# Kernel optimization log

Hardware: AMD Instinct MI355X
Metric: run time of the kernel (lower is better)

## Reference

```python
import jax, jax.numpy as jnp
import numpy as np

N_NODES = 65536
N_EDGES = 524288
N_GRAPHS = 512
G_NODES = 10000
NUM_DISEASES = 2000
IN_DIM = 128
HID = 256  # 2 * IN_DIM (z_emb concat feat)
D_FEAT = 512
C_FEAT = 512
MAX_Z = 4000


def setup_inputs() -> dict:
    key = jax.random.key(0)
    ks = jax.random.split(key, 20)
    rn = lambda k, shape: jax.random.normal(k, shape, dtype=jnp.float32) * 0.05
    return {
        "z": jax.random.randint(ks[0], (N_NODES,), 0, MAX_Z),
        "node_id": jnp.sort(jax.random.randint(ks[1], (N_NODES,), 0, G_NODES)),
        "src": jax.random.randint(ks[2], (N_EDGES,), 0, N_NODES),
        "dst": jax.random.randint(ks[3], (N_EDGES,), 0, N_NODES),
        "graph_ids": jnp.sort(jax.random.randint(ks[4], (N_NODES,), 0, N_GRAPHS)),
        "z_table": rn(ks[5], (MAX_Z, IN_DIM)),
        "d_feat_tab": rn(ks[6], (G_NODES, D_FEAT)),
        "c_feat_tab": rn(ks[7], (G_NODES, C_FEAT)),
        "Wd": rn(ks[8], (D_FEAT, IN_DIM)),
        "Wc": rn(ks[9], (C_FEAT, IN_DIM)),
        "gin_W1": rn(ks[10], (HID, HID)), "gin_b1": jnp.zeros((HID,), jnp.float32),
        "gin_W2": rn(ks[11], (HID, HID)), "gin_b2": jnp.zeros((HID,), jnp.float32),
        "sage_Wself": rn(ks[12], (HID, HID)),
        "sage_Wneigh": rn(ks[13], (HID, HID)),
        "sage_b": jnp.zeros((HID,), jnp.float32),
        "lin1_W": rn(ks[14], (HID, HID)), "lin1_b": jnp.zeros((HID,), jnp.float32),
        "lin2_W": rn(ks[15], (HID, 1)), "lin2_b": jnp.zeros((1,), jnp.float32),
    }


def reference(z, node_id, src, dst, graph_ids, z_table, d_feat_tab, c_feat_tab,
              Wd, Wc, gin_W1, gin_b1, gin_W2, gin_b2,
              sage_Wself, sage_Wneigh, sage_b, lin1_W, lin1_b, lin2_W, lin2_b):
    # --- input feature construction (Model.forward) ---
    z_emb = z_table[z]                               # [N, IN_DIM]
    d_proj = d_feat_tab[node_id] @ Wd                # d_fc (bias=False)
    c_proj = c_feat_tab[node_id] @ Wc                # c_fc (bias=False)
    disease = (node_id <= NUM_DISEASES)[:, None]
    # node_id is sorted -> masked concat order == node order
    feat = jnp.where(disease, d_proj, c_proj)        # [N, IN_DIM]
    x = jnp.concatenate([z_emb, feat], axis=1)       # [N, HID]
    # --- GINConv: sum aggregation, eps=0, mlp = Lin->ReLU->Lin ---
    agg = jax.ops.segment_sum(x[src], dst, num_segments=N_NODES)
    h = x + agg
    h = jax.nn.relu(h @ gin_W1 + gin_b1) @ gin_W2 + gin_b2
    # --- SAGEConv('mean'): fc_self(h) + fc_neigh(mean_neighbors) + bias ---
    deg = jax.ops.segment_sum(jnp.ones((N_EDGES,), h.dtype), dst, num_segments=N_NODES)
    mean_n = jax.ops.segment_sum(h[src], dst, num_segments=N_NODES) / jnp.maximum(deg, 1.0)[:, None]
    h = h @ sage_Wself + mean_n @ sage_Wneigh + sage_b
    # --- per-graph max pooling readout ---
    g = jax.ops.segment_max(h, graph_ids, num_segments=N_GRAPHS, indices_are_sorted=True)
    g = jnp.where(jnp.isfinite(g), g, 0.0)           # guard empty graphs
    # --- head: Linear -> ReLU -> (dropout p=0, eval) -> Linear ---
    h = jax.nn.relu(g @ lin1_W + lin1_b)
    return h @ lin2_W + lin2_b                       # [N_GRAPHS, 1]
```

## Files before the change

### kernel.cpp

```cpp
#include <hip/hip_runtime.h>
#include <hip/hip_bf16.h>

#define N_NODES     65536
#define N_EDGES     524288
#define N_GRAPHS    512
#define G_NODES_N   10000
#define NUM_DIS     2000
#define IN_DIM      128
#define HID         256
#define D_FEAT      512
#define MAX_Z       4000
#define POOL_SPLIT  8

typedef _Float16 half8 __attribute__((ext_vector_type(8)));
typedef float    f32x4 __attribute__((ext_vector_type(4)));

typedef __attribute__((address_space(1))) const void as1_void;
typedef __attribute__((address_space(3))) void       as3_void;

__global__ __launch_bounds__(256) void prep_kernel(
    const float* __restrict__ Ws, const float* __restrict__ Wn,
    const float* __restrict__ Wd, const float* __restrict__ Wc,
    const float* __restrict__ W1, const float* __restrict__ W2,
    const float* __restrict__ z_table,
    const int* __restrict__ z, const int* __restrict__ node_id,
    _Float16* __restrict__ WsT, _Float16* __restrict__ WnT,
    _Float16* __restrict__ WdT, _Float16* __restrict__ WcT,
    _Float16* __restrict__ W12P, _Float16* __restrict__ zt16,
    int2* __restrict__ zn2, int* __restrict__ cnt, int* __restrict__ flags)
{
    const int b = blockIdx.x;
    const int tid = threadIdx.x;
    if (b < 64) {
        __shared__ float tile[64][65];
        const float* W; _Float16* T; int K, N, k0, n0;
        if (b < 32) {
            const int mat = b >> 4, t = b & 15;
            K = HID; N = HID; k0 = (t >> 2) * 64; n0 = (t & 3) * 64;
            W = (mat == 0) ? Ws : Wn;
            T = (mat == 0) ? WsT : WnT;
        } else {
            const int bb = b - 32;
            const int mat = bb >> 4, t = bb & 15;
            K = D_FEAT; N = IN_DIM; k0 = (t >> 1) * 64; n0 = (t & 1) * 64;
            W = (mat == 0) ? Wd : Wc;
            T = (mat == 0) ? WdT : WcT;
        }
        const int tx = tid & 63, ty = tid >> 6;
        #pragma unroll
        for (int r = 0; r < 64; r += 4)
            tile[r + ty][tx] = W[(size_t)(k0 + r + ty) * N + n0 + tx];
        __syncthreads();
        #pragma unroll
        for (int c = 0; c < 64; c += 4)
            T[(size_t)(n0 + c + ty) * K + k0 + tx] = (_Float16)tile[tx][c + ty];
    } else if (b < 576) {
        const int bb = b - 64;
        const int mat = bb >> 8;
        const int k = bb & 255;
        const int n = tid;
        const float* W = mat ? W2 : W1;
        const float v = W[(size_t)k * HID + n];
        const size_t idx = (size_t)(mat * 8 + (k >> 5)) * 8192
                         + (size_t)((((k >> 3) & 3) * 256 + n) * 8 + (k & 7));
        W12P[idx] = (_Float16)v;
    } else if (b < 826) {
        const size_t base = ((size_t)(b - 576) * 256 + tid) * 8;
        const float4 f0 = *(const float4*)(z_table + base);
        const float4 f1 = *(const float4*)(z_table + base + 4);
        half8 h;
        h[0]=(_Float16)f0.x; h[1]=(_Float16)f0.y; h[2]=(_Float16)f0.z; h[3]=(_Float16)f0.w;
        h[4]=(_Float16)f1.x; h[5]=(_Float16)f1.y; h[6]=(_Float16)f1.z; h[7]=(_Float16)f1.w;
        *(half8*)(zt16 + base) = h;
    } else if (b < 890) {
        const int base = (b - 826) * 1024 + tid * 4;
        *(int4*)(cnt + base) = make_int4(0, 0, 0, 0);
        if (b == 826 && tid < 128) flags[tid] = 0;
    } else {
        const int i = (b - 890) * 256 + tid;
        zn2[i] = make_int2(z[i], node_id[i]);
    }
}

__global__ __launch_bounds__(256) void proj_hist_kernel(
    const float* __restrict__ dtab, const float* __restrict__ ctab,
    const _Float16* __restrict__ WdT, const _Float16* __restrict__ WcT,
    _Float16* __restrict__ proj,
    const int* __restrict__ dst, int* __restrict__ cnt)
{
    const int blk = blockIdx.x;
    if (blk >= 79) {
        const int e = (blk - 79) * 256 + threadIdx.x;
        if (e < N_EDGES) atomicAdd(&cnt[dst[e]], 1);
        return;
    }
    __shared__ _Float16 Alds[128 * 40];
    __shared__ _Float16 Blds[128 * 40];
    const float* tab; const _Float16* WT; int base, M, bm;
    if (blk < 16) { tab = dtab; WT = WdT; base = 0;           M = NUM_DIS + 1;             bm = blk * 128; }
    else          { tab = ctab; WT = WcT; base = NUM_DIS + 1; M = G_NODES_N - NUM_DIS - 1; bm = (blk - 16) * 128; }
    const int tid  = threadIdx.x;
    const int wave = tid >> 6, lane = tid & 63;
    const int q    = lane >> 4, l16 = lane & 15;
    const int mbase = (wave & 1) * 64, nbase = (wave >> 1) * 64;
    const int r = tid >> 1, s = tid & 1;

    f32x4 acc[4][4] = {};

    for (int kc = 0; kc < 16; ++kc) {
        const int k0 = kc * 32;
        const int arow = min(bm + r, M - 1);
        const float* gA = tab + (size_t)(base + arow) * D_FEAT + k0 + s * 16;
        const _Float16* gB = WT + (size_t)r * D_FEAT + k0 + s * 16;
        const float4 f0 = ((const float4*)gA)[0];
        const float4 f1 = ((const float4*)gA)[1];
        const float4 f2 = ((const float4*)gA)[2];
        const float4 f3 = ((const float4*)gA)[3];
        const half8 hb0 = *(const half8*)gB;
        const half8 hb1 = *(const half8*)(gB + 8);
        half8 h0, h1;
        h0[0]=(_Float16)f0.x; h0[1]=(_Float16)f0.y; h0[2]=(_Float16)f0.z; h0[3]=(_Float16)f0.w;
        h0[4]=(_Float16)f1.x; h0[5]=(_Float16)f1.y; h0[6]=(_Float16)f1.z; h0[7]=(_Float16)f1.w;
        h1[0]=(_Float16)f2.x; h1[1]=(_Float16)f2.y; h1[2]=(_Float16)f2.z; h1[3]=(_Float16)f2.w;
        h1[4]=(_Float16)f3.x; h1[5]=(_Float16)f3.y; h1[6]=(_Float16)f3.z; h1[7]=(_Float16)f3.w;
        __syncthreads();
        *(half8*)&Alds[r * 40 + s * 16]     = h0;
        *(half8*)&Alds[r * 40 + s * 16 + 8] = h1;
        *(half8*)&Blds[r * 40 + s * 16]     = hb0;
        *(half8*)&Blds[r * 40 + s * 16 + 8] = hb1;
        __syncthreads();
        half8 a[4], b[4];
        #pragma unroll
        for (int i = 0; i < 4; ++i)
            a[i] = *(const half8*)&Alds[(mbase + i * 16 + l16) * 40 + q * 8];
        #pragma unroll
        for (int j = 0; j < 4; ++j)
            b[j] = *(const half8*)&Blds[(nbase + j * 16 + l16) * 40 + q * 8];
        #pragma unroll
        for (int i = 0; i < 4; ++i)
            #pragma unroll
            for (int j = 0; j < 4; ++j)
                acc[i][j] = __builtin_amdgcn_mfma_f32_16x16x32_f16(a[i], b[j], acc[i][j], 0, 0, 0);
    }

    #pragma unroll
    for (int j = 0; j < 4; ++j) {
        const int colg = nbase + j * 16 + l16;
        #pragma unroll
        for (int i = 0; i < 4; ++i) {
            #pragma unroll
            for (int rr = 0; rr < 4; ++rr) {
                const int row = bm + mbase + i * 16 + q * 4 + rr;
                if (row < M)
                    proj[(size_t)(base + row) * IN_DIM + colg] = (_Float16)acc[i][j][rr];
            }
        }
    }
}

__global__ __launch_bounds__(256) void scan_fused_kernel(
    const int* __restrict__ cnt, int* __restrict__ row_ptr,
    int* __restrict__ fill, int* __restrict__ flags)
{
    __shared__ int a[256], b[256];
    __shared__ int sums[64];
    __shared__ int segbase;
    const int t = threadIdx.x;
    const int blk = blockIdx.x;
    const int base = blk * 1024 + t * 4;
    const int4 c = *(const int4*)(cnt + base);
    const int s = c.x + c.y + c.z + c.w;
    a[t] = s;
    __syncthreads();
    int* in = a; int* out = b;
    for (int off = 1; off < 256; off <<= 1) {
        out[t] = in[t] + ((t >= off) ? in[t - off] : 0);
        __syncthreads();
        int* tmp = in; in = out; out = tmp;
    }
    if (t == 0) {
        atomicExch(&flags[64 + blk], in[255]);
        __threadfence();
        atomicAdd(&flags[0], 1);
        while (atomicAdd(&flags[0], 0) < 64) {}
    }
    __syncthreads();
    if (t < 64) sums[t] = atomicAdd(&flags[64 + t], 0);
    __syncthreads();
    if (t == 0) {
        int pfx = 0;
        for (int i = 0; i < blk; ++i) pfx += sums[i];
        segbase = pfx;
        if (blk == 63) {
            int tot = pfx;
            for (int i = blk; i < 64; ++i) tot += sums[i];
            row_ptr[N_NODES] = tot;
        }
    }
    __syncthreads();
    const int run = in[t] - s + segbase;
    int4 r;
    r.x = run; r.y = run + c.x; r.z = r.y + c.y; r.w = r.z + c.z;
    *(int4*)(row_ptr + base) = r;
    *(int4*)(fill + base) = r;
}

__global__ __launch_bounds__(256) void scatter_kernel(
    const int* __restrict__ src, const int* __restrict__ dst,
    const int2* __restrict__ zn2,
    int* __restrict__ fill, int* __restrict__ col, int2* __restrict__ colzn)
{
    const int e = blockIdx.x * 256 + threadIdx.x;
    if (e < N_EDGES) {
        const int s = src[e];
        const int pos = atomicAdd(&fill[dst[e]], 1);
        col[pos] = s;
        colzn[pos] = zn2[s];
    }
}

__global__ __launch_bounds__(256) void gin_fused_kernel(
    const int* __restrict__ row_ptr, const int2* __restrict__ colzn,
    const int2* __restrict__ zn2,
    const _Float16* __restrict__ zt16, const _Float16* __restrict__ proj,
    const _Float16* __restrict__ W12P,
    const float* __restrict__ b1, const float* __restrict__ b2,
    _Float16* __restrict__ H)
{
    __shared__ _Float16 Apanel[64 * 264];
    __shared__ _Float16 Blds[8192];

    const int bm   = blockIdx.x * 64;
    const int tid  = threadIdx.x;
    const int wave = tid >> 6, lane = tid & 63;
    const int q    = lane >> 4, l16 = lane & 15;
    const int nbase = wave * 64;

    auto stage = [&](int c) {
        const _Float16* src = W12P + (size_t)c * 8192;
        #pragma unroll
        for (int tt = 0; tt < 4; ++tt) {
            const int seg = (wave * 4 + tt) * 64 + lane;
            __builtin_amdgcn_global_load_lds((as1_void*)(src + seg * 8),
                (as3_void*)&Blds[(wave * 4 + tt) * 64 * 8], 16, 0, 0);
        }
    };

    stage(0);

    {
        const int p = tid & 7;
        #pragma unroll 1
        for (int pass = 0; pass < 2; ++pass) {
            const int r  = (tid >> 3) + (pass << 5);
            const int gr = bm + r;
            const int beg = row_ptr[gr], end = row_ptr[gr + 1];
            float za[16], pa[16];
            {
                const int2 zn = zn2[gr];
                const half8* zp = (const half8*)(zt16 + (size_t)zn.x * IN_DIM + p * 16);
                const half8* pp = (const half8*)(proj + (size_t)zn.y * IN_DIM + p * 16);
                const half8 z0 = zp[0], z1 = zp[1], p0 = pp[0], p1 = pp[1];
                #pragma unroll
                for (int i = 0; i < 8; ++i) {
                    za[i] = (float)z0[i]; za[8 + i] = (float)z1[i];
                    pa[i] = (float)p0[i]; pa[8 + i] = (float)p1[i];
                }
            }
            int e = beg;
            for (; e + 4 <= end; e += 4) {
                const int2 znA = colzn[e],     znB = colzn[e + 1];
                const int2 znC = colzn[e + 2], znD = colzn[e + 3];
                const half8* zpA = (const half8*)(zt16 + (size_t)znA.x * IN_DIM + p * 16);
                const half8* ppA = (const half8*)(proj + (size_t)znA.y * IN_DIM + p * 16);
                const half8* zpB = (const half8*)(zt16 + (size_t)znB.x * IN_DIM + p * 16);
                const half8* ppB = (const half8*)(proj + (size_t)znB.y * IN_DIM + p * 16);
                const half8* zpC = (const half8*)(zt16 + (size_t)znC.x * IN_DIM + p * 16);
                const half8* ppC = (const half8*)(proj + (size_t)znC.y * IN_DIM + p * 16);
                const half8* zpD = (const half8*)(zt16 + (size_t)znD.x * IN_DIM + p * 16);
                const half8* ppD = (const half8*)(proj + (size_t)znD.y * IN_DIM + p * 16);
                const half8 zA0 = zpA[0], zA1 = zpA[1], pA0 = ppA[0], pA1 = ppA[1];
                const half8 zB0 = zpB[0], zB1 = zpB[1], pB0 = ppB[0], pB1 = ppB[1];
                const half8 zC0 = zpC[0], zC1 = zpC[1], pC0 = ppC[0], pC1 = ppC[1];
                const half8 zD0 = zpD[0], zD1 = zpD[1], pD0 = ppD[0], pD1 = ppD[1];
                #pragma unroll
                for (int i = 0; i < 8; ++i) {
                    za[i]     += ((float)zA0[i] + (float)zB0[i]) + ((float)zC0[i] + (float)zD0[i]);
                    za[8 + i] += ((float)zA1[i] + (float)zB1[i]) + ((float)zC1[i] + (float)zD1[i]);
                    pa[i]     += ((float)pA0[i] + (float)pB0[i]) + ((float)pC0[i] + (float)pD0[i]);
                    pa[8 + i] += ((float)pA1[i] + (float)pB1[i]) + ((float)pC1[i] + (float)pD1[i]);
                }
            }
            for (; e + 2 <= end; e += 2) {
                const int2 znA = colzn[e];
                const int2 znB = colzn[e + 1];
                const half8* zpA = (const half8*)(zt16 + (size_t)znA.x * IN_DIM + p * 16);
                const half8* ppA = (const half8*)(proj + (size_t)znA.y * IN_DIM + p * 16);
                const half8* zpB = (const half8*)(zt16 + (size_t)znB.x * IN_DIM + p * 16);
                const half8* ppB = (const half8*)(proj + (size_t)znB.y * IN_DIM + p * 16);
                const half8 zA0 = zpA[0], zA1 = zpA[1], pA0 = ppA[0], pA1 = ppA[1];
                const half8 zB0 = zpB[0], zB1 = zpB[1], pB0 = ppB[0], pB1 = ppB[1];
                #pragma unroll
                for (int i = 0; i < 8; ++i) {
                    za[i]     += (float)zA0[i] + (float)zB0[i];
                    za[8 + i] += (float)zA1[i] + (float)zB1[i];
                    pa[i]     += (float)pA0[i] + (float)pB0[i];
                    pa[8 + i] += (float)pA1[i] + (float)pB1[i];
                }
            }
            if (e < end) {
                const int2 zn = colzn[e];
                const half8* zp = (const half8*)(zt16 + (size_t)zn.x * IN_DIM + p * 16);
                const half8* pp = (const half8*)(proj + (size_t)zn.y * IN_DIM + p * 16);
                const half8 z0 = zp[0], z1 = zp[1], p0 = pp[0], p1 = pp[1];
                #pragma unroll
                for (int i = 0; i < 8; ++i) {
                    za[i] += (float)z0[i]; za[8 + i] += (float)z1[i];
                    pa[i] += (float)p0[i]; pa[8 + i] += (float)p1[i];
                }
            }
            half8 oz0, oz1, op0, op1;
            #pragma unroll
            for (int i = 0; i < 8; ++i) {
                oz0[i] = (_Float16)za[i];     oz1[i] = (_Float16)za[8 + i];
                op0[i] = (_Float16)pa[i];     op1[i] = (_Float16)pa[8 + i];
            }
            *(half8*)&Apanel[r * 264 + p * 16]           = oz0;
            *(half8*)&Apanel[r * 264 + p * 16 + 8]       = oz1;
            *(half8*)&Apanel[r * 264 + 128 + p * 16]     = op0;
            *(half8*)&Apanel[r * 264 + 128 + p * 16 + 8] = op1;
        }
    }
    __syncthreads();

    f32x4 acc[4][4] = {};
    for (int c = 0; c < 16; ++c) {
        if (c) {
            __syncthreads();
            stage(c);
            if (c == 8) {
                #pragma unroll
                for (int j = 0; j < 4; ++j) {
                    const int colg = nbase + j * 16 + l16;
                    const float bv = b1[colg];
                    #pragma unroll
                    for (int i = 0; i < 4; ++i)
                        #pragma unroll
                        for (int rr = 0; rr < 4; ++rr) {
                            const float v = fmaxf(acc[i][j][rr] + bv, 0.0f);
                            Apanel[(i * 16 + q * 4 + rr) * 264 + colg] = (_Float16)v;
                            acc[i][j][rr] = 0.0f;
                        }
                }
            }
            __syncthreads();
        }
        const int kl = (c & 7) * 32;
        half8 a[4], b[4];
        #pragma unroll
        for (int i = 0; i < 4; ++i)
            a[i] = *(const half8*)&Apanel[(i * 16 + l16) * 264 + kl + q * 8];
        #pragma unroll
        for (int j = 0; j < 4; ++j)
            b[j] = *(const half8*)&Blds[(q * 256 + nbase + j * 16 + l16) * 8];
        #pragma unroll
        for (int i = 0; i < 4; ++i)
            #pragma unroll
            for (int j = 0; j < 4; ++j)
                acc[i][j] = __builtin_amdgcn_mfma_f32_16x16x32_f16(a[i], b[j], acc[i][j], 0, 0, 0);
    }

    #pragma unroll
    for (int j = 0; j < 4; ++j) {
        const int colg = nbase + j * 16 + l16;
        const float bv = b2[colg];
        #pragma unroll
        for (int i = 0; i < 4; ++i)
            #pragma unroll
            for (int rr = 0; rr < 4; ++rr) {
                const int rowg = bm + i * 16 + q * 4 + rr;
                H[(size_t)rowg * HID + colg] = (_Float16)(acc[i][j][rr] + bv);
            }
    }
}

__global__ __launch_bounds__(256) void csr_agg_kernel(
    const int* __restrict__ row_ptr, const int* __restrict__ col,
    const _Float16* __restrict__ F, _Float16* __restrict__ OUT)
{
    const int t = blockIdx.x * 256 + threadIdx.x;
    const int d = t >> 5;
    const int q = t & 31;
    const int beg = row_ptr[d];
    const int end = row_ptr[d + 1];
    float acc[8] = {0.f,0.f,0.f,0.f,0.f,0.f,0.f,0.f};
    int e = beg;
    for (; e + 8 <= end; e += 8) {
        const int s0 = col[e],     s1 = col[e + 1];
        const int s2 = col[e + 2], s3 = col[e + 3];
        const int s4 = col[e + 4], s5 = col[e + 5];
        const int s6 = col[e + 6], s7 = col[e + 7];
        const half8 v0 = *(const half8*)(F + (size_t)s0 * HID + q * 8);
        const half8 v1 = *(const half8*)(F + (size_t)s1 * HID + q * 8);
        const half8 v2 = *(const half8*)(F + (size_t)s2 * HID + q * 8);
        const half8 v3 = *(const half8*)(F + (size_t)s3 * HID + q * 8);
        const half8 v4 = *(const half8*)(F + (size_t)s4 * HID + q * 8);
        const half8 v5 = *(const half8*)(F + (size_t)s5 * HID + q * 8);
        const half8 v6 = *(const half8*)(F + (size_t)s6 * HID + q * 8);
        const half8 v7 = *(const half8*)(F + (size_t)s7 * HID + q * 8);
        #pragma unroll
        for (int i = 0; i < 8; ++i)
            acc[i] += (((float)v0[i] + (float)v1[i]) + ((float)v2[i] + (float)v3[i]))
                    + (((float)v4[i] + (float)v5[i]) + ((float)v6[i] + (float)v7[i]));
    }
    for (; e + 4 <= end; e += 4) {
        const int s0 = col[e],     s1 = col[e + 1];
        const int s2 = col[e + 2], s3 = col[e + 3];
        const half8 v0 = *(const half8*)(F + (size_t)s0 * HID + q * 8);
        const half8 v1 = *(const half8*)(F + (size_t)s1 * HID + q * 8);
        const half8 v2 = *(const half8*)(F + (size_t)s2 * HID + q * 8);
        const half8 v3 = *(const half8*)(F + (size_t)s3 * HID + q * 8);
        #pragma unroll
        for (int i = 0; i < 8; ++i)
            acc[i] += ((float)v0[i] + (float)v1[i]) + ((float)v2[i] + (float)v3[i]);
    }
    for (; e < end; ++e) {
        const half8 v0 = *(const half8*)(F + (size_t)col[e] * HID + q * 8);
        #pragma unroll
        for (int i = 0; i < 8; ++i) acc[i] += (float)v0[i];
    }
    const float rs = 1.0f / fmaxf((float)(end - beg), 1.0f);
    half8 o;
    #pragma unroll
    for (int i = 0; i < 8; ++i) o[i] = (_Float16)(acc[i] * rs);
    *(half8*)(OUT + (size_t)d * HID + q * 8) = o;
}

__global__ __launch_bounds__(256) void mfma_gemm_kernel(
    const _Float16* __restrict__ A1, const _Float16* __restrict__ A2,
    const _Float16* __restrict__ B1T, const _Float16* __restrict__ B2T,
    const float* __restrict__ bias, _Float16* __restrict__ Ch)
{
    __shared__ _Float16 Alds[128 * 32];
    __shared__ _Float16 Blds[128 * 32];
    const int bm   = blockIdx.x * 128;
    const int bn   = blockIdx.y * 128;
    const int tid  = threadIdx.x;
    const int wave = tid >> 6, lane = tid & 63;
    const int q    = lane >> 4, l16 = lane & 15;
    const int mbase = (wave & 1) * 64, nbase = (wave >> 1) * 64;

    f32x4 acc[4][4] = {};

    for (int kc = 0; kc < 16; ++kc) {
        const int k0 = (kc & 7) * 32;
        const _Float16* Abase = (kc < 8) ? A1 : A2;
        const _Float16* Bbase = (kc < 8) ? B1T : B2T;
        __syncthreads();
        #pragma unroll
        for (int t = 0; t < 2; ++t) {
            const int i   = wave * 128 + t * 64 + lane;
            const int row = i >> 2, s = i & 3;
            const _Float16* gA = Abase + (size_t)(bm + row) * HID + k0 + s * 8;
            const _Float16* gB = Bbase + (size_t)(bn + row) * HID + k0 + s * 8;
            __builtin_amdgcn_global_load_lds(
                (as1_void*)gA, (as3_void*)&Alds[(wave * 128 + t * 64) * 8], 16, 0, 0);
            __builtin_amdgcn_global_load_lds(
                (as1_void*)gB, (as3_void*)&Blds[(wave * 128 + t * 64) * 8], 16, 0, 0);
        }
        __syncthreads();
        half8 a[4], b[4];
        #pragma unroll
        for (int i = 0; i < 4; ++i)
            a[i] = *(const half8*)&Alds[(mbase + i * 16 + l16) * 32 + q * 8];
        #pragma unroll
        for (int j = 0; j < 4; ++j)
            b[j] = *(const half8*)&Blds[(nbase + j * 16 + l16) * 32 + q * 8];
        #pragma unroll
        for (int i = 0; i < 4; ++i)
            #pragma unroll
            for (int j = 0; j < 4; ++j)
                acc[i][j] = __builtin_amdgcn_mfma_f32_16x16x32_f16(a[i], b[j], acc[i][j], 0, 0, 0);
    }

    #pragma unroll
    for (int j = 0; j < 4; ++j) {
        const int colg = bn + nbase + j * 16 + l16;
        const float bv = bias[colg];
        #pragma unroll
        for (int i = 0; i < 4; ++i) {
            #pragma unroll
            for (int rr = 0; rr < 4; ++rr) {
                const int rowg = bm + mbase + i * 16 + q * 4 + rr;
                Ch[(size_t)rowg * HID + colg] = (_Float16)(acc[i][j][rr] + bv);
            }
        }
    }
}

__global__ __launch_bounds__(256) void pool_part_kernel(
    const _Float16* __restrict__ H2, const int* __restrict__ gid,
    float* __restrict__ Gpart)
{
    const int g = blockIdx.y;
    const int sp = blockIdx.x;
    const int j = threadIdx.x;
    int lo = 0, hi = N_NODES;
    while (lo < hi) { const int mid = (lo + hi) >> 1; if (gid[mid] < g) lo = mid + 1; else hi = mid; }
    const int start = lo;
    hi = N_NODES;
    while (lo < hi) { const int mid = (lo + hi) >> 1; if (gid[mid] < g + 1) lo = mid + 1; else hi = mid; }
    const int end = lo;
    float m = -INFINITY;
    for (int i = start + sp; i < end; i += POOL_SPLIT)
        m = fmaxf(m, (float)H2[(size_t)i * HID + j]);
    Gpart[((size_t)g * POOL_SPLIT + sp) * HID + j] = m;
}

__global__ __launch_bounds__(256) void head_kernel(
    const float* __restrict__ Gpart,
    const float* __restrict__ W1, const float* __restrict__ b1,
    const float* __restrict__ W2, const float* __restrict__ b2,
    float* __restrict__ out)
{
    const int g = blockIdx.x;
    const int j = threadIdx.x;
    __shared__ float row[HID];
    __shared__ float red[HID];
    float m = -INFINITY;
    #pragma unroll
    for (int sp = 0; sp < POOL_SPLIT; ++sp)
        m = fmaxf(m, Gpart[((size_t)g * POOL_SPLIT + sp) * HID + j]);
    row[j] = (m == -INFINITY) ? 0.0f : m;
    __syncthreads();
    float acc = b1[j];
    #pragma unroll 8
    for (int k = 0; k < HID; ++k)
        acc = fmaf(row[k], W1[k * HID + j], acc);
    acc = fmaxf(acc, 0.f);
    red[j] = acc * W2[j];
    __syncthreads();
    for (int s = 128; s > 0; s >>= 1) {
        if (j < s) red[j] += red[j + s];
        __syncthreads();
    }
    if (j == 0) out[g] = red[0] + b2[0];
}

extern "C" void kernel_launch(void* const* d_in, const int* in_sizes, int n_in,
                              void* d_out, int out_size, void* d_ws, size_t ws_size,
                              hipStream_t stream)
{
    const int*   z         = (const int*)d_in[0];
    const int*   node_id   = (const int*)d_in[1];
    const int*   src       = (const int*)d_in[2];
    const int*   dst       = (const int*)d_in[3];
    const int*   graph_ids = (const int*)d_in[4];
    const float* z_table   = (const float*)d_in[5];
    const float* d_feat    = (const float*)d_in[6];
    const float* c_feat    = (const float*)d_in[7];
    const float* Wd        = (const float*)d_in[8];
    const float* Wc        = (const float*)d_in[9];
    const float* gin_W1    = (const float*)d_in[10];
    const float* gin_b1    = (const float*)d_in[11];
    const float* gin_W2    = (const float*)d_in[12];
    const float* gin_b2    = (const float*)d_in[13];
    const float* sage_Wself  = (const float*)d_in[14];
    const float* sage_Wneigh = (const float*)d_in[15];
    const float* sage_b    = (const float*)d_in[16];
    const float* lin1_W    = (const float*)d_in[17];
    const float* lin1_b    = (const float*)d_in[18];
    const float* lin2_W    = (const float*)d_in[19];
    const float* lin2_b    = (const float*)d_in[20];
    float* out = (float*)d_out;

    const size_t NH = (size_t)N_NODES * HID;
    char* wsb = (char*)d_ws;
    _Float16* Hh   = (_Float16*)wsb;                     wsb += NH * 2;
    _Float16* AGGh = (_Float16*)wsb;                     wsb += NH * 2;
    _Float16* H2h  = (_Float16*)wsb;                     wsb += NH * 2;
    _Float16* projh= (_Float16*)wsb;                     wsb += (size_t)G_NODES_N * IN_DIM * 2;
    _Float16* W12P = (_Float16*)wsb;                     wsb += 16 * 8192 * 2;
    _Float16* WsT  = (_Float16*)wsb;                     wsb += HID * HID * 2;
    _Float16* WnT  = (_Float16*)wsb;                     wsb += HID * HID * 2;
    _Float16* WdT  = (_Float16*)wsb;                     wsb += D_FEAT * IN_DIM * 2;
    _Float16* WcT  = (_Float16*)wsb;                     wsb += D_FEAT * IN_DIM * 2;
    _Float16* zt16 = (_Float16*)wsb;                     wsb += (size_t)MAX_Z * IN_DIM * 2;
    int2* zn2      = (int2*)wsb;                         wsb += (size_t)N_NODES * 8;
    int2* colzn    = (int2*)wsb;                         wsb += (size_t)N_EDGES * 8;
    float* Gpart   = (float*)wsb;                        wsb += (size_t)N_GRAPHS * POOL_SPLIT * HID * 4;
    int* row_ptr   = (int*)wsb;                          wsb += (N_NODES + 4) * 4;
    int* cnt       = (int*)wsb;                          wsb += N_NODES * 4;
    int* fill      = (int*)wsb;                          wsb += N_NODES * 4;
    int* col       = (int*)wsb;                          wsb += N_EDGES * 4;
    int* flags     = (int*)wsb;                          wsb += 128 * 4;

    prep_kernel<<<1146, 256, 0, stream>>>(
        sage_Wself, sage_Wneigh, Wd, Wc, gin_W1, gin_W2, z_table, z, node_id,
        WsT, WnT, WdT, WcT, W12P, zt16, zn2, cnt, flags);

    proj_hist_kernel<<<79 + N_EDGES / 256, 256, 0, stream>>>(
        d_feat, c_feat, WdT, WcT, projh, dst, cnt);

    scan_fused_kernel<<<64, 256, 0, stream>>>(cnt, row_ptr, fill, flags);
    scatter_kernel<<<N_EDGES / 256, 256, 0, stream>>>(src, dst, zn2, fill, col, colzn);

    gin_fused_kernel<<<N_NODES / 64, 256, 0, stream>>>(
        row_ptr, colzn, zn2, zt16, projh, W12P, gin_b1, gin_b2, Hh);

    csr_agg_kernel<<<(N_NODES * 32) / 256, 256, 0, stream>>>(row_ptr, col, Hh, AGGh);

    dim3 ggrid(N_NODES / 128, HID / 128);
    mfma_gemm_kernel<<<ggrid, 256, 0, stream>>>(Hh, AGGh, WsT, WnT, sage_b, H2h);

    dim3 pgrid(POOL_SPLIT, N_GRAPHS);
    pool_part_kernel<<<pgrid, 256, 0, stream>>>(H2h, graph_ids, Gpart);
    head_kernel<<<N_GRAPHS, 256, 0, stream>>>(Gpart, lin1_W, lin1_b, lin2_W, lin2_b, out);
}
```

Before: 360.6 us.

## Register-prefetch GEMM operand tiles and fuse pooling with MLP head

```diff
diff --git a/kernel.cpp b/kernel.cpp
--- a/kernel.cpp
+++ b/kernel.cpp
@@ -10,7 +10,6 @@
 #define HID         256
 #define D_FEAT      512
 #define MAX_Z       4000
-#define POOL_SPLIT  8
 
 typedef _Float16 half8 __attribute__((ext_vector_type(8)));
 typedef float    f32x4 __attribute__((ext_vector_type(4)));
@@ -235,18 +234,16 @@
     const int wave = tid >> 6, lane = tid & 63;
     const int q    = lane >> 4, l16 = lane & 15;
     const int nbase = wave * 64;
-
-    auto stage = [&](int c) {
-        const _Float16* src = W12P + (size_t)c * 8192;
+    const int sb   = wave * 256 + lane;
+
+    {
         #pragma unroll
         for (int tt = 0; tt < 4; ++tt) {
             const int seg = (wave * 4 + tt) * 64 + lane;
-            __builtin_amdgcn_global_load_lds((as1_void*)(src + seg * 8),
+            __builtin_amdgcn_global_load_lds((as1_void*)(W12P + seg * 8),
                 (as3_void*)&Blds[(wave * 4 + tt) * 64 * 8], 16, 0, 0);
         }
-    };
-
-    stage(0);
+    }
 
     {
         const int p = tid & 7;
@@ -333,28 +330,18 @@
     }
     __syncthreads();
 
+    half8 pf0, pf1, pf2, pf3;
+    auto pfetch = [&](int c) {
+        const _Float16* s = W12P + (size_t)c * 8192 + (size_t)sb * 8;
+        pf0 = *(const half8*)(s);
+        pf1 = *(const half8*)(s + 512);
+        pf2 = *(const half8*)(s + 1024);
+        pf3 = *(const half8*)(s + 1536);
+    };
+    pfetch(1);
+
     f32x4 acc[4][4] = {};
     for (int c = 0; c < 16; ++c) {
-        if (c) {
-            __syncthreads();
-            stage(c);
-            if (c == 8) {
-                #pragma unroll
-                for (int j = 0; j < 4; ++j) {
-                    const int colg = nbase + j * 16 + l16;
-                    const float bv = b1[colg];
-                    #pragma unroll
-                    for (int i = 0; i < 4; ++i)
-                        #pragma unroll
-                        for (int rr = 0; rr < 4; ++rr) {
-                            const float v = fmaxf(acc[i][j][rr] + bv, 0.0f);
-                            Apanel[(i * 16 + q * 4 + rr) * 264 + colg] = (_Float16)v;
-                            acc[i][j][rr] = 0.0f;
-                        }
-                }
-            }
-            __syncthreads();
-        }
         const int kl = (c & 7) * 32;
         half8 a[4], b[4];
         #pragma unroll
@@ -368,6 +355,29 @@
             #pragma unroll
             for (int j = 0; j < 4; ++j)
                 acc[i][j] = __builtin_amdgcn_mfma_f32_16x16x32_f16(a[i], b[j], acc[i][j], 0, 0, 0);
+        if (c == 15) break;
+        __syncthreads();
+        *(half8*)&Blds[sb * 8]         = pf0;
+        *(half8*)&Blds[(sb + 64) * 8]  = pf1;
+        *(half8*)&Blds[(sb + 128) * 8] = pf2;
+        *(half8*)&Blds[(sb + 192) * 8] = pf3;
+        if (c == 7) {
+            #pragma unroll
+            for (int j = 0; j < 4; ++j) {
+                const int colg = nbase + j * 16 + l16;
+                const float bv = b1[colg];
+                #pragma unroll
+                for (int i = 0; i < 4; ++i)
+                    #pragma unroll
+                    for (int rr = 0; rr < 4; ++rr) {
+                        const float v = fmaxf(acc[i][j][rr] + bv, 0.0f);
+                        Apanel[(i * 16 + q * 4 + rr) * 264 + colg] = (_Float16)v;
+                        acc[i][j][rr] = 0.0f;
+                    }
+            }
+        }
+        if (c < 14) pfetch(c + 2);
+        __syncthreads();
     }
 
     #pragma unroll
@@ -450,24 +460,32 @@
     const int q    = lane >> 4, l16 = lane & 15;
     const int mbase = (wave & 1) * 64, nbase = (wave >> 1) * 64;
 
+    const int i0 = wave * 128 + lane;
+    const int i1 = i0 + 64;
+    const int r0 = i0 >> 2, s0 = i0 & 3;
+    const int r1 = i1 >> 2, s1 = i1 & 3;
+
+    half8 pa0, pa1, pb0, pb1;
+    auto pfetch = [&](int kc) {
+        const int k0 = (kc & 7) * 32;
+        const _Float16* Ab = (kc < 8) ? A1 : A2;
+        const _Float16* Bb = (kc < 8) ? B1T : B2T;
+        pa0 = *(const half8*)(Ab + (size_t)(bm + r0) * HID + k0 + s0 * 8);
+        pa1 = *(const half8*)(Ab + (size_t)(bm + r1) * HID + k0 + s1 * 8);
+        pb0 = *(const half8*)(Bb + (size_t)(bn + r0) * HID + k0 + s0 * 8);
+        pb1 = *(const half8*)(Bb + (size_t)(bn + r1) * HID + k0 + s1 * 8);
+    };
+    pfetch(0);
+
     f32x4 acc[4][4] = {};
 
     for (int kc = 0; kc < 16; ++kc) {
-        const int k0 = (kc & 7) * 32;
-        const _Float16* Abase = (kc < 8) ? A1 : A2;
-        const _Float16* Bbase = (kc < 8) ? B1T : B2T;
-        __syncthreads();
-        #pragma unroll
-        for (int t = 0; t < 2; ++t) {
-            const int i   = wave * 128 + t * 64 + lane;
-            const int row = i >> 2, s = i & 3;
-            const _Float16* gA = Abase + (size_t)(bm + row) * HID + k0 + s * 8;
-            const _Float16* gB = Bbase + (size_t)(bn + row) * HID + k0 + s * 8;
-            __builtin_amdgcn_global_load_lds(
-                (as1_void*)gA, (as3_void*)&Alds[(wave * 128 + t * 64) * 8], 16, 0, 0);
-            __builtin_amdgcn_global_load_lds(
-                (as1_void*)gB, (as3_void*)&Blds[(wave * 128 + t * 64) * 8], 16, 0, 0);
-        }
+        __syncthreads();
+        *(half8*)&Alds[i0 * 8] = pa0;
+        *(half8*)&Alds[i1 * 8] = pa1;
+        *(half8*)&Blds[i0 * 8] = pb0;
+        *(half8*)&Blds[i1 * 8] = pb1;
+        if (kc < 15) pfetch(kc + 1);
         __syncthreads();
         half8 a[4], b[4];
         #pragma unroll
@@ -498,39 +516,41 @@
     }
 }
 
-__global__ __launch_bounds__(256) void pool_part_kernel(
+__global__ __launch_bounds__(256) void pool_head_kernel(
     const _Float16* __restrict__ H2, const int* __restrict__ gid,
-    float* __restrict__ Gpart)
-{
-    const int g = blockIdx.y;
-    const int sp = blockIdx.x;
-    const int j = threadIdx.x;
+    const float* __restrict__ W1, const float* __restrict__ b1,
+    const float* __restrict__ W2, const float* __restrict__ b2,
+    float* __restrict__ out)
+{
+    const int g = blockIdx.x;
+    const int tid = threadIdx.x;
     int lo = 0, hi = N_NODES;
     while (lo < hi) { const int mid = (lo + hi) >> 1; if (gid[mid] < g) lo = mid + 1; else hi = mid; }
     const int start = lo;
     hi = N_NODES;
     while (lo < hi) { const int mid = (lo + hi) >> 1; if (gid[mid] < g + 1) lo = mid + 1; else hi = mid; }
     const int end = lo;
-    float m = -INFINITY;
-    for (int i = start + sp; i < end; i += POOL_SPLIT)
-        m = fmaxf(m, (float)H2[(size_t)i * HID + j]);
-    Gpart[((size_t)g * POOL_SPLIT + sp) * HID + j] = m;
-}
-
-__global__ __launch_bounds__(256) void head_kernel(
-    const float* __restrict__ Gpart,
-    const float* __restrict__ W1, const float* __restrict__ b1,
-    const float* __restrict__ W2, const float* __restrict__ b2,
-    float* __restrict__ out)
-{
-    const int g = blockIdx.x;
-    const int j = threadIdx.x;
+
+    const int rowofs = tid >> 5;
+    const int q = tid & 31;
+    float m8[8];
+    #pragma unroll
+    for (int k = 0; k < 8; ++k) m8[k] = -INFINITY;
+    for (int i = start + rowofs; i < end; i += 8) {
+        const half8 v = *(const half8*)(H2 + (size_t)i * HID + q * 8);
+        #pragma unroll
+        for (int k = 0; k < 8; ++k) m8[k] = fmaxf(m8[k], (float)v[k]);
+    }
+    __shared__ float part[8][256];
+    #pragma unroll
+    for (int k = 0; k < 8; ++k) part[rowofs][q * 8 + k] = m8[k];
+    __syncthreads();
     __shared__ float row[HID];
     __shared__ float red[HID];
-    float m = -INFINITY;
+    const int j = tid;
+    float m = part[0][j];
     #pragma unroll
-    for (int sp = 0; sp < POOL_SPLIT; ++sp)
-        m = fmaxf(m, Gpart[((size_t)g * POOL_SPLIT + sp) * HID + j]);
+    for (int r = 1; r < 8; ++r) m = fmaxf(m, part[r][j]);
     row[j] = (m == -INFINITY) ? 0.0f : m;
     __syncthreads();
     float acc = b1[j];
@@ -588,7 +608,6 @@
     _Float16* zt16 = (_Float16*)wsb;                     wsb += (size_t)MAX_Z * IN_DIM * 2;
     int2* zn2      = (int2*)wsb;                         wsb += (size_t)N_NODES * 8;
     int2* colzn    = (int2*)wsb;                         wsb += (size_t)N_EDGES * 8;
-    float* Gpart   = (float*)wsb;                        wsb += (size_t)N_GRAPHS * POOL_SPLIT * HID * 4;
     int* row_ptr   = (int*)wsb;                          wsb += (N_NODES + 4) * 4;
     int* cnt       = (int*)wsb;                          wsb += N_NODES * 4;
     int* fill      = (int*)wsb;                          wsb += N_NODES * 4;
@@ -613,7 +632,6 @@
     dim3 ggrid(N_NODES / 128, HID / 128);
     mfma_gemm_kernel<<<ggrid, 256, 0, stream>>>(Hh, AGGh, WsT, WnT, sage_b, H2h);
 
-    dim3 pgrid(POOL_SPLIT, N_GRAPHS);
-    pool_part_kernel<<<pgrid, 256, 0, stream>>>(H2h, graph_ids, Gpart);
-    head_kernel<<<N_GRAPHS, 256, 0, stream>>>(Gpart, lin1_W, lin1_b, lin2_W, lin2_b, out);
-}
+    pool_head_kernel<<<N_GRAPHS, 256, 0, stream>>>(
+        H2h, graph_ids, lin1_W, lin1_b, lin2_W, lin2_b, out);
+}
```

Result: faster. 343.9 us (-4.6%).
